# Performance work log

Hardware: AMD Instinct MI355X
Metric: run time of the kernel (lower is better)

The kernel has to match this reference:

```python
import jax, jax.numpy as jnp
import numpy as np

DIM = 2048
H = 16
HKV = 4
D = DIM // H          # 128 head_dim
ROPE_BASE = 10000.0
TRAIN_SEQ_LEN = 1024
EPS = float(np.finfo(np.float32).eps)  # torch F.rms_norm default eps


def setup_inputs() -> dict:
    key = jax.random.key(0)
    ks = jax.random.split(key, 6)
    B, T = 2, 2048
    return {
        "x": jax.random.normal(ks[0], (B, T, DIM), jnp.float32),
        "q_w": jax.random.normal(ks[1], (DIM, DIM), jnp.float32) * 0.02,
        "k_w": jax.random.normal(ks[2], (HKV * D, DIM), jnp.float32) * 0.02,
        "v_w": jax.random.normal(ks[3], (HKV * D, DIM), jnp.float32) * 0.02,
        "out_w": jax.random.normal(ks[4], (DIM, DIM), jnp.float32) * 0.02,
        "q_gain": jnp.ones((H,), jnp.float32),
    }


def _rope_tables(T, dtype):
    rd = D  # rope_dims == head_dim (rope_dims=0 in module)
    if T > TRAIN_SEQ_LEN:
        scale = T / TRAIN_SEQ_LEN
        base = ROPE_BASE * scale ** (rd / (rd - 2))
    else:
        base = ROPE_BASE
    inv_freq = 1.0 / base ** (np.arange(0, rd, 2, dtype=np.float32) / rd)
    t = np.arange(T, dtype=np.float32)
    freqs = np.outer(t, inv_freq)  # [T, rd/2]
    cos = jnp.asarray(np.cos(freqs), dtype)[None, :, None, :]  # [1,T,1,rd/2]
    sin = jnp.asarray(np.sin(freqs), dtype)[None, :, None, :]
    return cos, sin


def _rms_norm(x):
    var = jnp.mean(jnp.square(x), axis=-1, keepdims=True)
    return x * jax.lax.rsqrt(var + EPS)


def _apply_rotary(x, cos, sin):
    half = x.shape[-1] // 2
    x1, x2 = x[..., :half], x[..., half:]
    return jnp.concatenate((x1 * cos + x2 * sin, -x1 * sin + x2 * cos), axis=-1)


def reference(x, q_w, k_w, v_w, out_w, q_gain):
    B, T, dim = x.shape
    q = (x @ q_w.T).reshape(B, T, H, D)
    k = (x @ k_w.T).reshape(B, T, HKV, D)
    v = (x @ v_w.T).reshape(B, T, HKV, D)
    q = _rms_norm(q)
    k = _rms_norm(k)
    cos, sin = _rope_tables(T, q.dtype)
    q = _apply_rotary(q, cos, sin)
    k = _apply_rotary(k, cos, sin)
    q = q * q_gain[None, None, :, None]
    rep = H // HKV
    k_r = jnp.repeat(k, rep, axis=2)  # [B,T,H,D]
    v_r = jnp.repeat(v, rep, axis=2)
    scores = jnp.einsum('bqhd,bkhd->bhqk', q, k_r) / jnp.sqrt(jnp.asarray(D, q.dtype))
    causal = jnp.tril(jnp.ones((T, T), bool))
    scores = jnp.where(causal[None, None], scores, jnp.asarray(-jnp.inf, scores.dtype))
    p = jax.nn.softmax(scores, axis=-1)
    y = jnp.einsum('bhqk,bkhd->bqhd', p, v_r).reshape(B, T, dim)
    return y @ out_w.T
```

## Files before the change

kernel.cpp:

```cpp
#include <hip/hip_runtime.h>
#include <hip/hip_bf16.h>

typedef __bf16 bf16x8 __attribute__((ext_vector_type(8)));
typedef unsigned short u16x8 __attribute__((ext_vector_type(8)));
typedef float f32x4 __attribute__((ext_vector_type(4)));
typedef __hip_bfloat16 bf16;

#define GLOAD_LDS16(g, l)                                               \
  __builtin_amdgcn_global_load_lds(                                     \
      (__attribute__((address_space(1))) void*)(void*)(g),              \
      (__attribute__((address_space(3))) void*)(void*)(l), 16, 0, 0)

__global__ __launch_bounds__(256) void cvt_all(
    const float4* __restrict__ x,  const float4* __restrict__ qw,
    const float4* __restrict__ kw, const float4* __restrict__ vw,
    const float4* __restrict__ ow,
    ushort4* __restrict__ xb,  ushort4* __restrict__ qwb,
    ushort4* __restrict__ kwb, ushort4* __restrict__ vwb,
    ushort4* __restrict__ owb)
{
  const int i = blockIdx.x * 256 + threadIdx.x;
  const float4* s; ushort4* d; int off;
  if      (i < 2097152) { s = x;  d = xb;  off = i; }
  else if (i < 3145728) { s = qw; d = qwb; off = i - 2097152; }
  else if (i < 3407872) { s = kw; d = kwb; off = i - 3145728; }
  else if (i < 3670016) { s = vw; d = vwb; off = i - 3407872; }
  else                  { s = ow; d = owb; off = i - 3670016; }
  float4 v = s[off];
  bf16 b0 = __float2bfloat16(v.x), b1 = __float2bfloat16(v.y);
  bf16 b2 = __float2bfloat16(v.z), b3 = __float2bfloat16(v.w);
  ushort4 o;
  o.x = *(unsigned short*)&b0; o.y = *(unsigned short*)&b1;
  o.z = *(unsigned short*)&b2; o.w = *(unsigned short*)&b3;
  d[off] = o;
}

__device__ __forceinline__ void store_out(bf16* p, float v)  { *p = __float2bfloat16(v); }
__device__ __forceinline__ void store_out(float* p, float v) { *p = v; }

template <typename OutT, int LD, int KLEN>
__device__ __forceinline__ void gemm256_body(
    const bf16* __restrict__ Ag, const bf16* __restrict__ Wg, OutT* __restrict__ C,
    int bm, int bn, int N, bf16* As0, bf16* As1, bf16* Bs0, bf16* Bs1)
{
  constexpr int NT = KLEN / 64;
  const int tid   = threadIdx.x;
  const int lane  = tid & 63;
  const int w     = tid >> 6;
  const int wr    = w >> 2;
  const int wc    = w & 3;
  const int mfrag = lane & 15;
  const int quad  = lane >> 4;
  const int m7x16 = (mfrag & 7) << 4;

  auto stage_half = [&](const bf16* __restrict__ G, int grow0, int k0, bf16* dsthalf) {
#pragma unroll
    for (int l = 0; l < 2; ++l) {
      const int o    = l * 8192 + tid * 16;
      const int row  = o >> 7;
      const int slot = ((o >> 4) & 7) ^ (row & 7);
      const bf16* src = G + (size_t)(grow0 + row) * LD + k0 + slot * 8;
      GLOAD_LDS16(src, (char*)dsthalf + l * 8192 + w * 1024);
    }
  };

  stage_half(Ag, bm,       0, As0);
  stage_half(Ag, bm + 128, 0, As0 + 8192);
  stage_half(Wg, bn,       0, Bs0);
  stage_half(Wg, bn + 128, 0, Bs0 + 8192);
  if (NT > 1) {
    stage_half(Wg, bn,       64, Bs1);
    stage_half(Wg, bn + 128, 64, Bs1 + 8192);
    asm volatile("s_waitcnt vmcnt(4)" ::: "memory");
  } else {
    asm volatile("s_waitcnt vmcnt(0)" ::: "memory");
  }
  __builtin_amdgcn_s_barrier();

  f32x4 acc[8][4] = {};

  for (int t = 0; t < NT; ++t) {
    const char* Ab = (const char*)((t & 1) ? As1 : As0);
    const char* Bb = (const char*)((t & 1) ? Bs1 : Bs0);
    bf16* Asn  = (t & 1) ? As0 : As1;
    bf16* Bsn2 = (t & 1) ? Bs1 : Bs0;

    bf16x8 bfr[4][2];
#pragma unroll
    for (int ph = 0; ph < 4; ++ph) {
      if (ph == 0) {
#pragma unroll
        for (int j = 0; j < 4; ++j) {
          const int rn = wc * 64 + j * 16 + mfrag;
#pragma unroll
          for (int kh = 0; kh < 2; ++kh)
            bfr[j][kh] = *(const bf16x8*)(Bb + ((rn * 128 + kh * 64 + quad * 16) ^ m7x16));
        }
      }
      bf16x8 afr[2][2];
#pragma unroll
      for (int r = 0; r < 2; ++r) {
        const int ra = wr * 128 + (ph * 2 + r) * 16 + mfrag;
#pragma unroll
        for (int kh = 0; kh < 2; ++kh)
          afr[r][kh] = *(const bf16x8*)(Ab + ((ra * 128 + kh * 64 + quad * 16) ^ m7x16));
      }

      if (ph == 0 && t + 1 < NT) stage_half(Ag, bm,       (t + 1) * 64, Asn);
      if (ph == 1 && t + 1 < NT) stage_half(Ag, bm + 128, (t + 1) * 64, Asn + 8192);
      if (ph == 2 && t + 2 < NT) stage_half(Wg, bn,       (t + 2) * 64, Bsn2);
      if (ph == 3 && t + 2 < NT) stage_half(Wg, bn + 128, (t + 2) * 64, Bsn2 + 8192);

      __builtin_amdgcn_s_barrier();
      asm volatile("s_waitcnt lgkmcnt(0)" ::: "memory");
      __builtin_amdgcn_s_setprio(1);
#pragma unroll
      for (int r = 0; r < 2; ++r)
#pragma unroll
        for (int j = 0; j < 4; ++j)
#pragma unroll
          for (int kh = 0; kh < 2; ++kh)
            acc[ph * 2 + r][j] = __builtin_amdgcn_mfma_f32_16x16x32_bf16(
                afr[r][kh], bfr[j][kh], acc[ph * 2 + r][j], 0, 0, 0);
      __builtin_amdgcn_s_setprio(0);
      if (ph == 3) {
        if (t < NT - 2) asm volatile("s_waitcnt vmcnt(4)" ::: "memory");
        else            asm volatile("s_waitcnt vmcnt(0)" ::: "memory");
      }
      __builtin_amdgcn_s_barrier();
    }
  }

  const int rq = quad * 4;
#pragma unroll
  for (int i = 0; i < 8; ++i)
#pragma unroll
    for (int j = 0; j < 4; ++j)
#pragma unroll
      for (int r = 0; r < 4; ++r) {
        const int row = bm + wr * 128 + i * 16 + rq + r;
        const int col = bn + wc * 64 + j * 16 + mfrag;
        store_out(&C[(size_t)row * N + col], acc[i][j][r]);
      }
}

template <typename OutT, int LD, int KLEN>
__device__ __forceinline__ void gemm256x128_body(
    const bf16* __restrict__ Ag, const bf16* __restrict__ Wg, OutT* __restrict__ C,
    int bm, int bn, int N, bf16* As0, bf16* As1, bf16* Bs0, bf16* Bs1)
{
  constexpr int NT = KLEN / 64;
  const int tid   = threadIdx.x;
  const int lane  = tid & 63;
  const int w     = tid >> 6;
  const int wr    = w >> 2;
  const int wc    = w & 3;
  const int mfrag = lane & 15;
  const int quad  = lane >> 4;
  const int m7x16 = (mfrag & 7) << 4;

  auto stage_half = [&](const bf16* __restrict__ G, int grow0, int k0, bf16* dsthalf) {
#pragma unroll
    for (int l = 0; l < 2; ++l) {
      const int o    = l * 8192 + tid * 16;
      const int row  = o >> 7;
      const int slot = ((o >> 4) & 7) ^ (row & 7);
      const bf16* src = G + (size_t)(grow0 + row) * LD + k0 + slot * 8;
      GLOAD_LDS16(src, (char*)dsthalf + l * 8192 + w * 1024);
    }
  };

  stage_half(Ag, bm,       0, As0);
  stage_half(Ag, bm + 128, 0, As0 + 8192);
  stage_half(Wg, bn, 0, Bs0);
  stage_half(Wg, bn, 64, Bs1);
  asm volatile("s_waitcnt vmcnt(2)" ::: "memory");
  __builtin_amdgcn_s_barrier();

  f32x4 acc[8][2] = {};

  for (int t = 0; t < NT; ++t) {
    const char* Ab = (const char*)((t & 1) ? As1 : As0);
    const char* Bb = (const char*)((t & 1) ? Bs1 : Bs0);
    bf16* Asn  = (t & 1) ? As0 : As1;
    bf16* Bsn2 = (t & 1) ? Bs1 : Bs0;

    bf16x8 bfr[2][2];
#pragma unroll
    for (int ph = 0; ph < 4; ++ph) {
      if (ph == 0) {
#pragma unroll
        for (int j = 0; j < 2; ++j) {
          const int rn = wc * 32 + j * 16 + mfrag;
#pragma unroll
          for (int kh = 0; kh < 2; ++kh)
            bfr[j][kh] = *(const bf16x8*)(Bb + ((rn * 128 + kh * 64 + quad * 16) ^ m7x16));
        }
      }
      bf16x8 afr[2][2];
#pragma unroll
      for (int r = 0; r < 2; ++r) {
        const int ra = wr * 128 + (ph * 2 + r) * 16 + mfrag;
#pragma unroll
        for (int kh = 0; kh < 2; ++kh)
          afr[r][kh] = *(const bf16x8*)(Ab + ((ra * 128 + kh * 64 + quad * 16) ^ m7x16));
      }

      if (ph == 0 && t + 1 < NT) stage_half(Ag, bm,       (t + 1) * 64, Asn);
      if (ph == 1 && t + 1 < NT) stage_half(Ag, bm + 128, (t + 1) * 64, Asn + 8192);
      if (ph == 2 && t + 2 < NT) stage_half(Wg, bn,       (t + 2) * 64, Bsn2);

      __builtin_amdgcn_s_barrier();
      asm volatile("s_waitcnt lgkmcnt(0)" ::: "memory");
      __builtin_amdgcn_s_setprio(1);
#pragma unroll
      for (int r = 0; r < 2; ++r)
#pragma unroll
        for (int j = 0; j < 2; ++j)
#pragma unroll
          for (int kh = 0; kh < 2; ++kh)
            acc[ph * 2 + r][j] = __builtin_amdgcn_mfma_f32_16x16x32_bf16(
                afr[r][kh], bfr[j][kh], acc[ph * 2 + r][j], 0, 0, 0);
      __builtin_amdgcn_s_setprio(0);
      if (ph == 3) {
        if (t < NT - 2) asm volatile("s_waitcnt vmcnt(2)" ::: "memory");
        else            asm volatile("s_waitcnt vmcnt(0)" ::: "memory");
      }
      __builtin_amdgcn_s_barrier();
    }
  }

  const int rq = quad * 4;
#pragma unroll
  for (int i = 0; i < 8; ++i)
#pragma unroll
    for (int j = 0; j < 2; ++j)
#pragma unroll
      for (int r = 0; r < 4; ++r) {
        const int row = bm + wr * 128 + i * 16 + rq + r;
        const int col = bn + wc * 32 + j * 16 + mfrag;
        store_out(&C[(size_t)row * N + col], acc[i][j][r]);
      }
}

__global__ __launch_bounds__(512, 2) void gemm_qkv256(
    const bf16* __restrict__ X,  const bf16* __restrict__ Wq,
    const bf16* __restrict__ Wk, const bf16* __restrict__ Wv,
    bf16* __restrict__ Qo, bf16* __restrict__ Ko, bf16* __restrict__ Vo)
{
  __shared__ alignas(16) bf16 As[2][16384];
  __shared__ alignas(16) bf16 Bs[2][16384];
  const int orig = blockIdx.y * 12 + blockIdx.x;
  const int swz  = (orig & 7) * 24 + (orig >> 3);
  const int bx   = swz % 12;
  const int by   = swz / 12;
  const bf16* W; bf16* C; int N, bn;
  if (bx < 8)       { W = Wq; C = Qo; N = 2048; bn = bx * 256; }
  else if (bx < 10) { W = Wk; C = Ko; N = 512;  bn = (bx - 8) * 256; }
  else              { W = Wv; C = Vo; N = 512;  bn = (bx - 10) * 256; }
  gemm256_body<bf16, 2048, 2048>(X, W, C, by * 256, bn, N,
                                 As[0], As[1], Bs[0], Bs[1]);
}

__global__ __launch_bounds__(512, 2) void gemm_out256(
    const bf16* __restrict__ A, const bf16* __restrict__ W, float* __restrict__ C)
{
  __shared__ alignas(16) bf16 As[2][16384];
  __shared__ alignas(16) bf16 Bs[2][8192];
  const int orig = blockIdx.y * 16 + blockIdx.x;
  const int swz  = (orig & 7) * 32 + (orig >> 3);
  const int bx   = swz & 15;
  const int by   = swz >> 4;
  gemm256x128_body<float, 2048, 2048>(A, W, C, by * 256, bx * 128, 2048,
                                      As[0], As[1], Bs[0], Bs[1]);
}

__device__ __forceinline__ void rope_row(
    bf16* __restrict__ buf, const float* __restrict__ gain,
    int nh, float scale, int row)
{
  const int j = threadIdx.x & 63;
  const int bt = row / nh;
  const int h  = row - bt * nh;
  const int t  = bt & 2047;
  bf16* p = buf + (size_t)bt * (nh * 128) + h * 128;

  float x1 = __bfloat162float(p[j]);
  float x2 = __bfloat162float(p[j + 64]);
  float ss = x1 * x1 + x2 * x2;
#pragma unroll
  for (int off = 32; off > 0; off >>= 1) ss += __shfl_xor(ss, off, 64);
  const float rinv = rsqrtf(ss * (1.0f / 128.0f) + 1.1920928955078125e-07f);
  const float g = gain ? gain[h] : 1.0f;
  const float s = rinv * g * scale;

  const float inv_freq = exp2f(-(float)j * (14.3035853954f / 64.0f));
  const float fr = (float)t * inv_freq;
  const float cs = cosf(fr), sn = sinf(fr);
  p[j]      = __float2bfloat16(s * (x1 * cs + x2 * sn));
  p[j + 64] = __float2bfloat16(s * (x2 * cs - x1 * sn));
}

__global__ __launch_bounds__(256) void postqkv(
    bf16* __restrict__ qb, bf16* __restrict__ kb,
    const unsigned short* __restrict__ vb, unsigned short* __restrict__ vtb,
    const float* __restrict__ gain)
{
  const int bx = blockIdx.x;
  if (bx < 16384) {
    rope_row(qb, gain, 16, 0.08838834764831845f, bx * 4 + (threadIdx.x >> 6));
  } else if (bx < 20480) {
    rope_row(kb, nullptr, 4, 1.0f, (bx - 16384) * 4 + (threadIdx.x >> 6));
  } else {
    const int idx = (bx - 20480) * 256 + threadIdx.x;
    const int t  = idx & 4095;
    const int dc = idx >> 12;
    u16x8 v = *(const u16x8*)(vb + (size_t)t * 512 + dc * 8);
#pragma unroll
    for (int j = 0; j < 8; ++j)
      vtb[(size_t)(dc * 8 + j) * 4096 + t] = v[j];
  }
}

__global__ __launch_bounds__(256) void flash_attn(
    const bf16* __restrict__ Q, const bf16* __restrict__ Kg,
    const bf16* __restrict__ Vtg, bf16* __restrict__ Y)
{
  __shared__ bf16 Ks[2][64 * 128];
  __shared__ bf16 Vs[2][128 * 64];
  __shared__ bf16 Ps[4][16 * 64];

  const int tid = threadIdx.x, lane = tid & 63, w = tid >> 6;
  const int p = blockIdx.x & 15, bh = blockIdx.x >> 4;
  const int h = bh & 15, b = bh >> 4, kvh = h >> 2;
  const int mfrag = lane & 15, quad = lane >> 4;
  const int m7 = mfrag & 7;

  auto stage_k = [&](int kt, int s) {
#pragma unroll
    for (int g = 0; g < 4; ++g) {
      const int o = g * 4096 + w * 1024 + lane * 16;
      const int r = o >> 8, c = (o >> 4) & 15;
      const int cs = (c & 8) | ((c ^ (r & 7)) & 7);
      const bf16* src = Kg + ((size_t)(b * 2048 + kt * 64 + r)) * 512 + kvh * 128 + cs * 8;
      GLOAD_LDS16(src, (char*)&Ks[s][0] + g * 4096 + w * 1024);
    }
  };
  auto stage_v = [&](int kt, int s) {
#pragma unroll
    for (int g = 0; g < 4; ++g) {
      const int o = g * 4096 + w * 1024 + lane * 16;
      const int r = o >> 7, c = (o >> 4) & 7;
      const int cs = (c ^ (r & 7)) & 7;
      const bf16* src = Vtg + ((size_t)(kvh * 128 + r)) * 4096 + b * 2048 + kt * 64 + cs * 8;
      GLOAD_LDS16(src, (char*)&Vs[s][0] + g * 4096 + w * 1024);
    }
  };

  stage_k(0, 0);
  stage_v(0, 0);
  int sb = 0;
  bf16* psw = &Ps[w][0];

  for (int phase = 0; phase < 2; ++phase) {
    const int qt = phase ? p : 31 - p;

    bf16x8 qf[4];
    const bf16* qrow = Q + ((size_t)(b * 2048 + qt * 64 + w * 16 + mfrag)) * 2048 + h * 128;
#pragma unroll
    for (int c = 0; c < 4; ++c) qf[c] = *(const bf16x8*)(qrow + c * 32 + quad * 8);

    f32x4 oacc[8] = {};
    float l_lane[4] = {0.f, 0.f, 0.f, 0.f};
    const int q_base = qt * 64 + w * 16 + quad * 4;

    for (int kt = 0; kt <= qt; ++kt) {
      __syncthreads();
      const bool last = (phase == 1) && (kt == qt);
      if (!last) {
        const int nk = kt < qt ? kt + 1 : 0;
        stage_k(nk, sb ^ 1);
        stage_v(nk, sb ^ 1);
      }

      f32x4 sc[4] = {};
      __builtin_amdgcn_s_setprio(1);
#pragma unroll
      for (int kc = 0; kc < 4; ++kc) {
        const bf16* krow = &Ks[sb][0] + (kc * 16 + mfrag) * 128;
#pragma unroll
        for (int c = 0; c < 4; ++c) {
          const int G = 4 * c + quad;
          const int cs = (G & 8) | ((G ^ m7) & 7);
          bf16x8 kf = *(const bf16x8*)(krow + cs * 8);
          sc[kc] = __builtin_amdgcn_mfma_f32_16x16x32_bf16(qf[c], kf, sc[kc], 0, 0, 0);
        }
      }
      __builtin_amdgcn_s_setprio(0);

      if (kt == qt) {
        const int kcol0 = kt * 64 + mfrag;
#pragma unroll
        for (int kc = 0; kc < 4; ++kc)
#pragma unroll
          for (int r = 0; r < 4; ++r)
            if (kcol0 + kc * 16 > q_base + r) sc[kc][r] = -1e30f;
      }

#pragma unroll
      for (int kc = 0; kc < 4; ++kc)
#pragma unroll
        for (int r = 0; r < 4; ++r) {
          const float pv = __expf(sc[kc][r] - 14.0f);
          l_lane[r] += pv;
          const int q = quad * 4 + r;
          const int slot = ((2 * kc + (mfrag >> 3)) ^ (q & 7)) & 7;
          psw[q * 64 + slot * 8 + m7] = __float2bfloat16(pv);
        }

      __builtin_amdgcn_s_setprio(1);
#pragma unroll
      for (int kh = 0; kh < 2; ++kh) {
        const int Gp = 4 * kh + quad;
        const int sl = (Gp ^ m7) & 7;
        bf16x8 pf = *(const bf16x8*)(psw + mfrag * 64 + sl * 8);
#pragma unroll
        for (int dc = 0; dc < 8; ++dc) {
          bf16x8 vf = *(const bf16x8*)(&Vs[sb][0] + (dc * 16 + mfrag) * 64 + sl * 8);
          oacc[dc] = __builtin_amdgcn_mfma_f32_16x16x32_bf16(pf, vf, oacc[dc], 0, 0, 0);
        }
      }
      __builtin_amdgcn_s_setprio(0);
      sb ^= 1;
    }

#pragma unroll
    for (int r = 0; r < 4; ++r) {
      float l = l_lane[r];
      l += __shfl_xor(l, 1, 64);
      l += __shfl_xor(l, 2, 64);
      l += __shfl_xor(l, 4, 64);
      l += __shfl_xor(l, 8, 64);
      const float linv = 1.0f / l;
      const size_t row = (size_t)(b * 2048 + q_base + r);
#pragma unroll
      for (int dc = 0; dc < 8; ++dc)
        Y[row * 2048 + h * 128 + dc * 16 + mfrag] = __float2bfloat16(oacc[dc][r] * linv);
    }
  }
}

extern "C" void kernel_launch(void* const* d_in, const int* in_sizes, int n_in,
                              void* d_out, int out_size, void* d_ws, size_t ws_size,
                              hipStream_t stream)
{
  const float* x      = (const float*)d_in[0];
  const float* q_w    = (const float*)d_in[1];
  const float* k_w    = (const float*)d_in[2];
  const float* v_w    = (const float*)d_in[3];
  const float* o_w    = (const float*)d_in[4];
  const float* q_gain = (const float*)d_in[5];
  float* out = (float*)d_out;

  char* ws = (char*)d_ws;
  bf16* xb  = (bf16*)(ws);
  bf16* yb  = (bf16*)(ws);
  bf16* qwb = (bf16*)(ws + (16u << 20));
  bf16* vtb = (bf16*)(ws + (16u << 20));
  bf16* owb = (bf16*)(ws + (24u << 20));
  bf16* kwb = (bf16*)(ws + (32u << 20));
  bf16* vwb = (bf16*)(ws + (34u << 20));
  bf16* qb  = (bf16*)(ws + (36u << 20));
  bf16* kb  = (bf16*)(ws + (52u << 20));
  bf16* vb  = (bf16*)(ws + (56u << 20));

  cvt_all<<<dim3(18432), dim3(256), 0, stream>>>(
      (const float4*)x, (const float4*)q_w, (const float4*)k_w,
      (const float4*)v_w, (const float4*)o_w,
      (ushort4*)xb, (ushort4*)qwb, (ushort4*)kwb, (ushort4*)vwb, (ushort4*)owb);

  gemm_qkv256<<<dim3(12, 16), dim3(512), 0, stream>>>(xb, qwb, kwb, vwb, qb, kb, vb);

  postqkv<<<dim3(21504), dim3(256), 0, stream>>>(
      qb, kb, (const unsigned short*)vb, (unsigned short*)vtb, q_gain);

  flash_attn<<<dim3(512), dim3(256), 0, stream>>>(qb, kb, vtb, yb);

  gemm_out256<<<dim3(16, 16), dim3(512), 0, stream>>>(yb, owb, out);
}
```

Measured before the change: 312.8 us.

## Double query tile per block in flash attention to reuse K/V tiles

Each wave now processes two 16-row query fragments (128 query rows per block instead of 64), so every staged K and V tile in shared memory feeds twice as many MFMAs. The grid halves from 512 to 256 blocks, with causal pairing kept across 16 query tiles. This cuts K/V global-to-LDS traffic and synchronisation per unit of work, at the cost of more registers (two accumulator sets) and fewer blocks. On a GPU with many compute units that risks idle units and lower occupancy.

```diff
diff --git a/kernel.cpp b/kernel.cpp
--- a/kernel.cpp
+++ b/kernel.cpp
@@ -328,10 +328,10 @@
 {
   __shared__ bf16 Ks[2][64 * 128];
   __shared__ bf16 Vs[2][128 * 64];
-  __shared__ bf16 Ps[4][16 * 64];
+  __shared__ bf16 Ps[4][2][16 * 64];
 
   const int tid = threadIdx.x, lane = tid & 63, w = tid >> 6;
-  const int p = blockIdx.x & 15, bh = blockIdx.x >> 4;
+  const int p = blockIdx.x & 7, bh = blockIdx.x >> 3;
   const int h = bh & 15, b = bh >> 4, kvh = h >> 2;
   const int mfrag = lane & 15, quad = lane >> 4;
   const int m7 = mfrag & 7;
@@ -360,30 +360,37 @@
   stage_k(0, 0);
   stage_v(0, 0);
   int sb = 0;
-  bf16* psw = &Ps[w][0];
+  bf16* pswA = &Ps[w][0][0];
+  bf16* pswB = &Ps[w][1][0];
 
   for (int phase = 0; phase < 2; ++phase) {
-    const int qt = phase ? p : 31 - p;
-
-    bf16x8 qf[4];
-    const bf16* qrow = Q + ((size_t)(b * 2048 + qt * 64 + w * 16 + mfrag)) * 2048 + h * 128;
-#pragma unroll
-    for (int c = 0; c < 4; ++c) qf[c] = *(const bf16x8*)(qrow + c * 32 + quad * 8);
-
-    f32x4 oacc[8] = {};
-    float l_lane[4] = {0.f, 0.f, 0.f, 0.f};
-    const int q_base = qt * 64 + w * 16 + quad * 4;
-
-    for (int kt = 0; kt <= qt; ++kt) {
+    const int qt = phase ? p : 15 - p;
+    const int nkt = 2 * qt + 2;
+
+    const bf16* qrowA = Q + ((size_t)(b * 2048 + qt * 128 + w * 32 + mfrag)) * 2048 + h * 128;
+    const bf16* qrowB = qrowA + 16 * 2048;
+    bf16x8 qfA[4], qfB[4];
+#pragma unroll
+    for (int c = 0; c < 4; ++c) {
+      qfA[c] = *(const bf16x8*)(qrowA + c * 32 + quad * 8);
+      qfB[c] = *(const bf16x8*)(qrowB + c * 32 + quad * 8);
+    }
+
+    f32x4 oaccA[8] = {}, oaccB[8] = {};
+    float lA[4] = {0.f, 0.f, 0.f, 0.f}, lB[4] = {0.f, 0.f, 0.f, 0.f};
+    const int qbA = qt * 128 + w * 32 + quad * 4;
+    const int qbB = qbA + 16;
+
+    for (int kt = 0; kt < nkt; ++kt) {
       __syncthreads();
-      const bool last = (phase == 1) && (kt == qt);
+      const bool last = (phase == 1) && (kt == nkt - 1);
       if (!last) {
-        const int nk = kt < qt ? kt + 1 : 0;
+        const int nk = (kt < nkt - 1) ? kt + 1 : 0;
         stage_k(nk, sb ^ 1);
         stage_v(nk, sb ^ 1);
       }
 
-      f32x4 sc[4] = {};
+      f32x4 scA[4] = {}, scB[4] = {};
       __builtin_amdgcn_s_setprio(1);
 #pragma unroll
       for (int kc = 0; kc < 4; ++kc) {
@@ -393,29 +400,35 @@
           const int G = 4 * c + quad;
           const int cs = (G & 8) | ((G ^ m7) & 7);
           bf16x8 kf = *(const bf16x8*)(krow + cs * 8);
-          sc[kc] = __builtin_amdgcn_mfma_f32_16x16x32_bf16(qf[c], kf, sc[kc], 0, 0, 0);
+          scA[kc] = __builtin_amdgcn_mfma_f32_16x16x32_bf16(qfA[c], kf, scA[kc], 0, 0, 0);
+          scB[kc] = __builtin_amdgcn_mfma_f32_16x16x32_bf16(qfB[c], kf, scB[kc], 0, 0, 0);
         }
       }
       __builtin_amdgcn_s_setprio(0);
 
-      if (kt == qt) {
+      if (kt >= 2 * qt) {
         const int kcol0 = kt * 64 + mfrag;
 #pragma unroll
         for (int kc = 0; kc < 4; ++kc)
 #pragma unroll
-          for (int r = 0; r < 4; ++r)
-            if (kcol0 + kc * 16 > q_base + r) sc[kc][r] = -1e30f;
+          for (int r = 0; r < 4; ++r) {
+            if (kcol0 + kc * 16 > qbA + r) scA[kc][r] = -1e30f;
+            if (kcol0 + kc * 16 > qbB + r) scB[kc][r] = -1e30f;
+          }
       }
 
 #pragma unroll
       for (int kc = 0; kc < 4; ++kc)
 #pragma unroll
         for (int r = 0; r < 4; ++r) {
-          const float pv = __expf(sc[kc][r] - 14.0f);
-          l_lane[r] += pv;
           const int q = quad * 4 + r;
           const int slot = ((2 * kc + (mfrag >> 3)) ^ (q & 7)) & 7;
-          psw[q * 64 + slot * 8 + m7] = __float2bfloat16(pv);
+          const float pvA = __expf(scA[kc][r] - 14.0f);
+          lA[r] += pvA;
+          pswA[q * 64 + slot * 8 + m7] = __float2bfloat16(pvA);
+          const float pvB = __expf(scB[kc][r] - 14.0f);
+          lB[r] += pvB;
+          pswB[q * 64 + slot * 8 + m7] = __float2bfloat16(pvB);
         }
 
       __builtin_amdgcn_s_setprio(1);
@@ -423,11 +436,13 @@
       for (int kh = 0; kh < 2; ++kh) {
         const int Gp = 4 * kh + quad;
         const int sl = (Gp ^ m7) & 7;
-        bf16x8 pf = *(const bf16x8*)(psw + mfrag * 64 + sl * 8);
+        bf16x8 pfA = *(const bf16x8*)(pswA + mfrag * 64 + sl * 8);
+        bf16x8 pfB = *(const bf16x8*)(pswB + mfrag * 64 + sl * 8);
 #pragma unroll
         for (int dc = 0; dc < 8; ++dc) {
           bf16x8 vf = *(const bf16x8*)(&Vs[sb][0] + (dc * 16 + mfrag) * 64 + sl * 8);
-          oacc[dc] = __builtin_amdgcn_mfma_f32_16x16x32_bf16(pf, vf, oacc[dc], 0, 0, 0);
+          oaccA[dc] = __builtin_amdgcn_mfma_f32_16x16x32_bf16(pfA, vf, oaccA[dc], 0, 0, 0);
+          oaccB[dc] = __builtin_amdgcn_mfma_f32_16x16x32_bf16(pfB, vf, oaccB[dc], 0, 0, 0);
         }
       }
       __builtin_amdgcn_s_setprio(0);
@@ -436,16 +451,27 @@
 
 #pragma unroll
     for (int r = 0; r < 4; ++r) {
-      float l = l_lane[r];
-      l += __shfl_xor(l, 1, 64);
-      l += __shfl_xor(l, 2, 64);
-      l += __shfl_xor(l, 4, 64);
-      l += __shfl_xor(l, 8, 64);
-      const float linv = 1.0f / l;
-      const size_t row = (size_t)(b * 2048 + q_base + r);
+      float la = lA[r];
+      la += __shfl_xor(la, 1, 64);
+      la += __shfl_xor(la, 2, 64);
+      la += __shfl_xor(la, 4, 64);
+      la += __shfl_xor(la, 8, 64);
+      const float linvA = 1.0f / la;
+      const size_t rowA = (size_t)(b * 2048 + qbA + r);
 #pragma unroll
       for (int dc = 0; dc < 8; ++dc)
-        Y[row * 2048 + h * 128 + dc * 16 + mfrag] = __float2bfloat16(oacc[dc][r] * linv);
+        Y[rowA * 2048 + h * 128 + dc * 16 + mfrag] = __float2bfloat16(oaccA[dc][r] * linvA);
+
+      float lb = lB[r];
+      lb += __shfl_xor(lb, 1, 64);
+      lb += __shfl_xor(lb, 2, 64);
+      lb += __shfl_xor(lb, 4, 64);
+      lb += __shfl_xor(lb, 8, 64);
+      const float linvB = 1.0f / lb;
+      const size_t rowB = (size_t)(b * 2048 + qbB + r);
+#pragma unroll
+      for (int dc = 0; dc < 8; ++dc)
+        Y[rowB * 2048 + h * 128 + dc * 16 + mfrag] = __float2bfloat16(oaccB[dc][r] * linvB);
     }
   }
 }
@@ -484,7 +510,7 @@
   postqkv<<<dim3(21504), dim3(256), 0, stream>>>(
       qb, kb, (const unsigned short*)vb, (unsigned short*)vtb, q_gain);
 
-  flash_attn<<<dim3(512), dim3(256), 0, stream>>>(qb, kb, vtb, yb);
+  flash_attn<<<dim3(256), dim3(256), 0, stream>>>(qb, kb, vtb, yb);
 
   gemm_out256<<<dim3(16, 16), dim3(512), 0, stream>>>(yb, owb, out);
 }
```

Measured after the change: 305.1 us. 1.03x faster.
